# Performance work log

Measured on AMD Instinct MI355X. Metric: run time of the kernel, lower is better.

## Reference

```python
import jax, jax.numpy as jnp
import numpy as np

B, LQ, LK, NF = 8, 8192, 1024, 64


def setup_inputs() -> dict:
    key = jax.random.key(0)
    k1, k2, k3, k4, k5 = jax.random.split(key, 5)
    x = jax.random.normal(k1, (B, LQ, NF), dtype=jnp.float32)
    kv = jax.random.normal(k2, (B, LK, NF), dtype=jnp.float32)
    # 1x1 submanifold convolutions == per-point linear maps (no bias)
    scale = 1.0 / np.sqrt(NF)
    Wq = jax.random.normal(k3, (NF, NF), dtype=jnp.float32) * scale
    Wk = jax.random.normal(k4, (NF, NF), dtype=jnp.float32) * scale
    Wv = jax.random.normal(k5, (NF, NF), dtype=jnp.float32) * scale
    return {"x": x, "kv": kv, "Wq": Wq, "Wk": Wk, "Wv": Wv}


def reference(x, kv, Wq, Wk, Wv):
    # q/k/v projections (1x1 convs on sparse features = dense matmuls)
    q = jnp.einsum("bqd,de->bqe", x, Wq)    # [B, LQ, NF]
    k = jnp.einsum("bkd,de->bke", kv, Wk)   # [B, LK, NF]
    v = jnp.einsum("bkd,de->bke", kv, Wv)   # [B, LK, NF]
    # per-batch (block-diagonal / ragged) attention: e = q k^T, softmax over keys, @ v
    scores = jnp.einsum("bqe,bke->bqk", q, k)        # [B, LQ, LK] (no scaling, as in source)
    attn = jax.nn.softmax(scores, axis=-1)
    out = jnp.einsum("bqk,bke->bqe", attn, v)        # [B, LQ, NF]
    return out
```

## Files before the change

### kernel.cpp

```cpp
#include <hip/hip_runtime.h>
#include <hip/hip_fp16.h>

constexpr int B_  = 8;
constexpr int LQ  = 8192;
constexpr int LK  = 1024;
constexpr int NF  = 64;

typedef _Float16 f16x8  __attribute__((ext_vector_type(8)));
typedef float    f32x16 __attribute__((ext_vector_type(16)));

#define MFMA32(a, b, c) __builtin_amdgcn_mfma_f32_32x32x16_f16((a), (b), (c), 0, 0, 0)

__device__ __forceinline__ f16x8 ldf(const _Float16* p) { return *(const f16x8*)p; }

__device__ __forceinline__ f16x8 ldfrag_f32(const float* row, int t, int h) {
  int off = 32 * (t >> 1) + 16 * (t & 1) + 4 * h;
  float4 r0 = *(const float4*)(row + off);
  float4 r1 = *(const float4*)(row + off + 8);
  f16x8 r;
  r[0] = (_Float16)r0.x; r[1] = (_Float16)r0.y; r[2] = (_Float16)r0.z; r[3] = (_Float16)r0.w;
  r[4] = (_Float16)r1.x; r[5] = (_Float16)r1.y; r[6] = (_Float16)r1.z; r[7] = (_Float16)r1.w;
  return r;
}

__device__ __forceinline__ f16x8 pk8(const f32x16 c, int u) {
  int b = u * 8;
  auto p0 = __builtin_amdgcn_cvt_pkrtz(c[b],     c[b + 1]);
  auto p1 = __builtin_amdgcn_cvt_pkrtz(c[b + 2], c[b + 3]);
  auto p2 = __builtin_amdgcn_cvt_pkrtz(c[b + 4], c[b + 5]);
  auto p3 = __builtin_amdgcn_cvt_pkrtz(c[b + 6], c[b + 7]);
  f16x8 r;
  r[0] = p0[0]; r[1] = p0[1]; r[2] = p1[0]; r[3] = p1[1];
  r[4] = p2[0]; r[5] = p2[1]; r[6] = p3[0]; r[7] = p3[1];
  return r;
}

__device__ __forceinline__ int w_src_idx(int idx) {
  int chunk = idx >> 9, r9 = idx & 511;
  int lane_ = r9 >> 3, j = r9 & 7;
  int m32 = lane_ & 31, h = lane_ >> 5;
  int tt = chunk & 3;
  int din  = 32 * (tt >> 1) + 16 * (tt & 1) + 4 * h + 8 * (j >> 2) + (j & 3);
  int dout = (chunk >> 2) * 32 + m32;
  return din * 64 + dout;
}

__device__ __forceinline__ void dma16(const _Float16* g, _Float16* l) {
  __builtin_amdgcn_global_load_lds(
      (const __attribute__((address_space(1))) unsigned int*)g,
      (__attribute__((address_space(3))) unsigned int*)l, 16, 0, 0);
}

__device__ __forceinline__ void tile_barrier() {
  asm volatile("s_waitcnt vmcnt(0)\n\ts_barrier" ::: "memory");
}

__global__ __launch_bounds__(256) void kv_proj_kernel(
    const float* __restrict__ kv, const float* __restrict__ Wk,
    const float* __restrict__ Wv, _Float16* __restrict__ KV) {
  __shared__ __align__(16) _Float16 wlds[8192];

  const int t    = threadIdx.x;
  const int wave = t >> 6, lane = t & 63, m32 = lane & 31, h = lane >> 5;
  const int bb   = blockIdx.x >> 3;
  const int kblk = blockIdx.x & 7;

#pragma unroll
  for (int i = 0; i < 16; ++i) {
    int idx = t + 256 * i;
    int s = w_src_idx(idx);
    wlds[idx]        = (_Float16)Wk[s];
    wlds[4096 + idx] = (_Float16)Wv[s];
  }

  const int key = kblk * 128 + wave * 32 + m32;
  const float* kvrow = kv + ((size_t)bb * LK + key) * NF;
  f16x8 kvf[4];
#pragma unroll
  for (int tt = 0; tt < 4; ++tt) kvf[tt] = ldfrag_f32(kvrow, tt, h);
  __syncthreads();

  const int T = bb * 16 + kblk * 2 + (wave >> 1);
  _Float16* tile = KV + (size_t)T * 8192;
  const int kb = wave & 1;

#pragma unroll
  for (int mb = 0; mb < 2; ++mb) {
    f32x16 C = {};
#pragma unroll
    for (int tt = 0; tt < 4; ++tt)
      C = MFMA32(ldf(&wlds[(mb * 4 + tt) * 512 + lane * 8]), kvf[tt], C);
#pragma unroll
    for (int u = 0; u < 2; ++u)
      *(f16x8*)(tile + ((size_t)(kb * 4 + 2 * mb + u)) * 512 + lane * 8) = pk8(C, u);
  }
#pragma unroll
  for (int nb = 0; nb < 2; ++nb) {
    f32x16 C = {};
#pragma unroll
    for (int tt = 0; tt < 4; ++tt)
      C = MFMA32(kvf[tt], ldf(&wlds[4096 + (nb * 4 + tt) * 512 + lane * 8]), C);
#pragma unroll
    for (int u = 0; u < 2; ++u)
      *(f16x8*)(tile + 4096 + ((size_t)(nb * 4 + 2 * kb + u)) * 512 + lane * 8) = pk8(C, u);
  }
}

__global__ __launch_bounds__(256, 1) void attn_kernel(
    const float* __restrict__ x, const float* __restrict__ Wq,
    const _Float16* __restrict__ KV, float* __restrict__ out) {
  __shared__ __align__(16) _Float16 lds[2 * 8192 + 4096];

  const int t    = threadIdx.x;
  const int wave = t >> 6, lane = t & 63, m32 = lane & 31, h = lane >> 5;
  const int b    = blockIdx.x >> 5;
  const int qw_base = (blockIdx.x & 31) * 256 + wave * 64;
  constexpr float LOG2E = 1.44269504088896f;

  _Float16* wq_l = lds + 16384;
#pragma unroll
  for (int i = 0; i < 16; ++i) {
    int idx = t + 256 * i;
    wq_l[idx] = (_Float16)(Wq[w_src_idx(idx)] * LOG2E);
  }

  const _Float16* KVb = KV + (size_t)b * 16 * 8192;
#pragma unroll
  for (int q = 0; q < 4; ++q) {
    int ch = wave * 4 + q;
    dma16(KVb + ch * 512 + lane * 8, lds + ch * 512);
  }
  __syncthreads();

  f16x8 qb[2][4];
  {
    f16x8 wa[2][4];
#pragma unroll
    for (int mb = 0; mb < 2; ++mb)
#pragma unroll
      for (int tt = 0; tt < 4; ++tt)
        wa[mb][tt] = ldf(&wq_l[(mb * 4 + tt) * 512 + lane * 8]);
#pragma unroll
    for (int s = 0; s < 2; ++s) {
      const float* xrow = x + ((size_t)b * LQ + qw_base + s * 32 + m32) * NF;
      f16x8 xf[4];
#pragma unroll
      for (int tt = 0; tt < 4; ++tt) xf[tt] = ldfrag_f32(xrow, tt, h);
#pragma unroll
      for (int mb = 0; mb < 2; ++mb) {
        f32x16 C = {};
#pragma unroll
        for (int tt = 0; tt < 4; ++tt) C = MFMA32(wa[mb][tt], xf[tt], C);
        qb[s][2 * mb]     = pk8(C, 0);
        qb[s][2 * mb + 1] = pk8(C, 1);
      }
    }
  }

  f16x8 ones;
#pragma unroll
  for (int j = 0; j < 8; ++j) ones[j] = (_Float16)1.0f;

  float  m_s[2] = {-1e30f, -1e30f};
  f32x16 lacc[2] = {};
  f32x16 oacc[2][2] = {};

  for (int tile = 0; tile < 16; ++tile) {
    tile_barrier();
    if (tile < 15) {
      const _Float16* nt = KVb + (size_t)(tile + 1) * 8192;
      _Float16* nb_ = lds + ((tile + 1) & 1) * 8192;
#pragma unroll
      for (int q = 0; q < 4; ++q) {
        int ch = wave * 4 + q;
        dma16(nt + ch * 512 + lane * 8, nb_ + ch * 512);
      }
    }
    const _Float16* tb = lds + (tile & 1) * 8192;

    f32x16 st[2][2] = {};
#pragma unroll
    for (int kb = 0; kb < 2; ++kb)
#pragma unroll
      for (int tt = 0; tt < 4; ++tt) {
        f16x8 a = ldf(tb + (size_t)(kb * 4 + tt) * 512 + lane * 8);
        st[0][kb] = MFMA32(a, qb[0][tt], st[0][kb]);
        st[1][kb] = MFMA32(a, qb[1][tt], st[1][kb]);
      }

    f16x8 pa[2][4];
#pragma unroll
    for (int s = 0; s < 2; ++s) {
      float tmax = st[s][0][0];
#pragma unroll
      for (int kb = 0; kb < 2; ++kb)
#pragma unroll
        for (int r = 1 - kb; r < 16; ++r) tmax = fmaxf(tmax, st[s][kb][r]);
      tmax = fmaxf(tmax, __shfl_xor(tmax, 32));

      if (__ballot(tmax > m_s[s]) != 0) {
        float mnew  = fmaxf(m_s[s], tmax);
        float alpha = __builtin_amdgcn_exp2f(m_s[s] - mnew);
        m_s[s] = mnew;
        float ar[16];
#pragma unroll
        for (int r = 0; r < 16; ++r)
          ar[r] = __shfl(alpha, (r & 3) + 8 * (r >> 2) + 4 * h);
#pragma unroll
        for (int r = 0; r < 16; ++r) {
          lacc[s][r]    *= ar[r];
          oacc[s][0][r] *= ar[r];
          oacc[s][1][r] *= ar[r];
        }
      }

#pragma unroll
      for (int kb = 0; kb < 2; ++kb)
#pragma unroll
        for (int r = 0; r < 16; ++r)
          st[s][kb][r] = __builtin_amdgcn_exp2f(st[s][kb][r] - m_s[s]);

#pragma unroll
      for (int kb = 0; kb < 2; ++kb) {
        pa[s][2 * kb]     = pk8(st[s][kb], 0);
        pa[s][2 * kb + 1] = pk8(st[s][kb], 1);
      }
#pragma unroll
      for (int tt = 0; tt < 4; ++tt) lacc[s] = MFMA32(pa[s][tt], ones, lacc[s]);
    }

#pragma unroll
    for (int nb = 0; nb < 2; ++nb)
#pragma unroll
      for (int tt = 0; tt < 4; ++tt) {
        f16x8 vb = ldf(tb + 4096 + (size_t)(nb * 4 + tt) * 512 + lane * 8);
        oacc[0][nb] = MFMA32(pa[0][tt], vb, oacc[0][nb]);
        oacc[1][nb] = MFMA32(pa[1][tt], vb, oacc[1][nb]);
      }
  }

#pragma unroll
  for (int s = 0; s < 2; ++s)
#pragma unroll
    for (int r = 0; r < 16; ++r) {
      float linv = 1.0f / lacc[s][r];
      int q_out = qw_base + s * 32 + (r & 3) + 8 * (r >> 2) + 4 * h;
      float* orow = out + ((size_t)b * LQ + q_out) * NF + m32;
      orow[0]  = oacc[s][0][r] * linv;
      orow[32] = oacc[s][1][r] * linv;
    }
}

extern "C" void kernel_launch(void* const* d_in, const int* in_sizes, int n_in,
                              void* d_out, int out_size, void* d_ws, size_t ws_size,
                              hipStream_t stream) {
  const float* x  = (const float*)d_in[0];
  const float* kv = (const float*)d_in[1];
  const float* Wq = (const float*)d_in[2];
  const float* Wk = (const float*)d_in[3];
  const float* Wv = (const float*)d_in[4];
  float* out = (float*)d_out;

  _Float16* KV = (_Float16*)d_ws;

  kv_proj_kernel<<<B_ * (LK / 128), 256, 0, stream>>>(kv, Wk, Wv, KV);
  attn_kernel<<<B_ * (LQ / 256), 256, 0, stream>>>(x, Wq, KV, out);
}
```

Before: 116.2 us.

## Split key range across two wave groups per block and merge softmax states

Attention blocks grow from 256 to 512 threads. Two groups of four waves each process half of the key tiles (8 tiles each) for the same 256 queries, with separate double-buffered LDS regions. At the end the partial max, row-sum and output accumulators from group 1 go through LDS and group 0 merges them flash-decoding style before writing. The aim is to halve the serial key loop per wave and raise occupancy, at the cost of more LDS, an extra merge phase and duplicated Q projection work in both groups.

```diff
diff --git a/kernel.cpp b/kernel.cpp
--- a/kernel.cpp
+++ b/kernel.cpp
@@ -106,29 +106,30 @@
   }
 }
 
-__global__ __launch_bounds__(256, 1) void attn_kernel(
+__global__ __launch_bounds__(512, 2) void attn_kernel(
     const float* __restrict__ x, const float* __restrict__ Wq,
     const _Float16* __restrict__ KV, float* __restrict__ out) {
-  __shared__ __align__(16) _Float16 lds[2 * 8192 + 4096];
+  __shared__ __align__(16) _Float16 lds[2][2][8192];
+  __shared__ __align__(16) _Float16 wq_l[4096];
 
   const int t    = threadIdx.x;
   const int wave = t >> 6, lane = t & 63, m32 = lane & 31, h = lane >> 5;
+  const int wq_i = wave & 3, wg = wave >> 2;
   const int b    = blockIdx.x >> 5;
-  const int qw_base = (blockIdx.x & 31) * 256 + wave * 64;
+  const int qw_base = (blockIdx.x & 31) * 256 + wq_i * 64;
   constexpr float LOG2E = 1.44269504088896f;
 
-  _Float16* wq_l = lds + 16384;
-#pragma unroll
-  for (int i = 0; i < 16; ++i) {
-    int idx = t + 256 * i;
+#pragma unroll
+  for (int i = 0; i < 8; ++i) {
+    int idx = t + 512 * i;
     wq_l[idx] = (_Float16)(Wq[w_src_idx(idx)] * LOG2E);
   }
 
-  const _Float16* KVb = KV + (size_t)b * 16 * 8192;
+  const _Float16* Kg = KV + ((size_t)b * 16 + wg * 8) * 8192;
 #pragma unroll
   for (int q = 0; q < 4; ++q) {
-    int ch = wave * 4 + q;
-    dma16(KVb + ch * 512 + lane * 8, lds + ch * 512);
+    int ch = wq_i * 4 + q;
+    dma16(Kg + ch * 512 + lane * 8, &lds[wg][0][ch * 512]);
   }
   __syncthreads();
 
@@ -165,18 +166,18 @@
   f32x16 lacc[2] = {};
   f32x16 oacc[2][2] = {};
 
-  for (int tile = 0; tile < 16; ++tile) {
+  for (int tile = 0; tile < 8; ++tile) {
     tile_barrier();
-    if (tile < 15) {
-      const _Float16* nt = KVb + (size_t)(tile + 1) * 8192;
-      _Float16* nb_ = lds + ((tile + 1) & 1) * 8192;
+    if (tile < 7) {
+      const _Float16* nt = Kg + (size_t)(tile + 1) * 8192;
+      _Float16* nb_ = &lds[wg][(tile + 1) & 1][0];
 #pragma unroll
       for (int q = 0; q < 4; ++q) {
-        int ch = wave * 4 + q;
+        int ch = wq_i * 4 + q;
         dma16(nt + ch * 512 + lane * 8, nb_ + ch * 512);
       }
     }
-    const _Float16* tb = lds + (tile & 1) * 8192;
+    const _Float16* tb = &lds[wg][tile & 1][0];
 
     f32x16 st[2][2] = {};
 #pragma unroll
@@ -239,16 +240,50 @@
       }
   }
 
-#pragma unroll
-  for (int s = 0; s < 2; ++s)
-#pragma unroll
-    for (int r = 0; r < 16; ++r) {
-      float linv = 1.0f / lacc[s][r];
-      int q_out = qw_base + s * 32 + (r & 3) + 8 * (r >> 2) + 4 * h;
-      float* orow = out + ((size_t)b * LQ + q_out) * NF + m32;
-      orow[0]  = oacc[s][0][r] * linv;
-      orow[32] = oacc[s][1][r] * linv;
-    }
+  float* mrg_m = (float*)&lds[0][0][0];
+  float* mrg_l = mrg_m + 256;
+  float* mrg_o = mrg_l + 4096;
+
+#pragma unroll
+  for (int s = 0; s < 2; ++s) {
+    __syncthreads();
+    if (wg == 1) {
+      mrg_m[wq_i * 64 + lane] = m_s[s];
+#pragma unroll
+      for (int r = 0; r < 16; ++r)
+        mrg_l[(wq_i * 16 + r) * 64 + lane] = lacc[s][r];
+#pragma unroll
+      for (int nb = 0; nb < 2; ++nb)
+#pragma unroll
+        for (int r = 0; r < 16; ++r)
+          mrg_o[(wq_i * 32 + nb * 16 + r) * 64 + lane] = oacc[s][nb][r];
+    }
+    __syncthreads();
+    if (wg == 0) {
+      float mh = mrg_m[wq_i * 64 + lane];
+      float mx = fmaxf(m_s[s], mh);
+      float al = __builtin_amdgcn_exp2f(m_s[s] - mx);
+      float ah = __builtin_amdgcn_exp2f(mh - mx);
+      float alr[16], ahr[16];
+#pragma unroll
+      for (int r = 0; r < 16; ++r) {
+        int src = (r & 3) + 8 * (r >> 2) + 4 * h;
+        alr[r] = __shfl(al, src);
+        ahr[r] = __shfl(ah, src);
+      }
+#pragma unroll
+      for (int r = 0; r < 16; ++r) {
+        float lh = mrg_l[(wq_i * 16 + r) * 64 + lane];
+        float linv = 1.0f / (alr[r] * lacc[s][r] + ahr[r] * lh);
+        int q_out = qw_base + s * 32 + (r & 3) + 8 * (r >> 2) + 4 * h;
+        float* orow = out + ((size_t)b * LQ + q_out) * NF + m32;
+        float o0 = alr[r] * oacc[s][0][r] + ahr[r] * mrg_o[(wq_i * 32 + r) * 64 + lane];
+        float o1 = alr[r] * oacc[s][1][r] + ahr[r] * mrg_o[(wq_i * 32 + 16 + r) * 64 + lane];
+        orow[0]  = o0 * linv;
+        orow[32] = o1 * linv;
+      }
+    }
+  }
 }
 
 extern "C" void kernel_launch(void* const* d_in, const int* in_sizes, int n_in,
@@ -264,5 +299,5 @@
   _Float16* KV = (_Float16*)d_ws;
 
   kv_proj_kernel<<<B_ * (LK / 128), 256, 0, stream>>>(kv, Wk, Wv, KV);
-  attn_kernel<<<B_ * (LQ / 256), 256, 0, stream>>>(x, Wq, KV, out);
-}
+  attn_kernel<<<B_ * (LQ / 256), 512, 0, stream>>>(x, Wq, KV, out);
+}
```

Result: faster. 111.9 us (-3.7%).

## Split keys across waves, drop online max, use bf16 P·V with LDS merge

Applied to the files above, without the earlier changes.

Restructures attention so each block handles 64 queries, with wave pairs splitting the key range and merging partial sums and outputs through LDS. Removes the running-max rescaling entirely, relying on bf16/fp32 exponent range to avoid overflow, and stores V and P in bf16. Launch bounds are raised to allow four blocks per CU. It trades numerical safety for large scores and precision of P and V for fewer VALU, shuffle and branch operations per tile.

```diff
diff --git a/kernel.cpp b/kernel.cpp
--- a/kernel.cpp
+++ b/kernel.cpp
@@ -6,12 +6,16 @@
 constexpr int LK  = 1024;
 constexpr int NF  = 64;
 
-typedef _Float16 f16x8  __attribute__((ext_vector_type(8)));
-typedef float    f32x16 __attribute__((ext_vector_type(16)));
-
-#define MFMA32(a, b, c) __builtin_amdgcn_mfma_f32_32x32x16_f16((a), (b), (c), 0, 0, 0)
+typedef _Float16     f16x8  __attribute__((ext_vector_type(8)));
+typedef short        s16x8  __attribute__((ext_vector_type(8)));
+typedef unsigned int u32x4  __attribute__((ext_vector_type(4)));
+typedef float        f32x16 __attribute__((ext_vector_type(16)));
+
+#define MFMA32F(a, b, c) __builtin_amdgcn_mfma_f32_32x32x16_f16((a), (b), (c), 0, 0, 0)
+#define MFMA32B(a, b, c) __builtin_amdgcn_mfma_f32_32x32x16_bf16((a), (b), (c), 0, 0, 0)
 
 __device__ __forceinline__ f16x8 ldf(const _Float16* p) { return *(const f16x8*)p; }
+__device__ __forceinline__ s16x8 ldb(const _Float16* p) { return *(const s16x8*)p; }
 
 __device__ __forceinline__ f16x8 ldfrag_f32(const float* row, int t, int h) {
   int off = 32 * (t >> 1) + 16 * (t & 1) + 4 * h;
@@ -35,6 +39,22 @@
   return r;
 }
 
+__device__ __forceinline__ unsigned int bpack(float a, float b) {
+  unsigned int ua = __builtin_bit_cast(unsigned int, a) + 0x8000u;
+  unsigned int ub = __builtin_bit_cast(unsigned int, b) + 0x8000u;
+  return __builtin_amdgcn_perm(ub, ua, 0x07060302u);
+}
+
+__device__ __forceinline__ s16x8 pk8b(const f32x16 c, int u) {
+  int b = u * 8;
+  u32x4 r;
+  r[0] = bpack(c[b],     c[b + 1]);
+  r[1] = bpack(c[b + 2], c[b + 3]);
+  r[2] = bpack(c[b + 4], c[b + 5]);
+  r[3] = bpack(c[b + 6], c[b + 7]);
+  return __builtin_bit_cast(s16x8, r);
+}
+
 __device__ __forceinline__ int w_src_idx(int idx) {
   int chunk = idx >> 9, r9 = idx & 511;
   int lane_ = r9 >> 3, j = r9 & 7;
@@ -80,175 +100,135 @@
   for (int tt = 0; tt < 4; ++tt) kvf[tt] = ldfrag_f32(kvrow, tt, h);
   __syncthreads();
 
-  const int T = bb * 16 + kblk * 2 + (wave >> 1);
-  _Float16* tile = KV + (size_t)T * 8192;
-  const int kb = wave & 1;
+  _Float16* base = KV + ((size_t)bb * 32 + kblk * 4 + wave) * 4096;
 
 #pragma unroll
   for (int mb = 0; mb < 2; ++mb) {
     f32x16 C = {};
 #pragma unroll
     for (int tt = 0; tt < 4; ++tt)
-      C = MFMA32(ldf(&wlds[(mb * 4 + tt) * 512 + lane * 8]), kvf[tt], C);
+      C = MFMA32F(ldf(&wlds[(mb * 4 + tt) * 512 + lane * 8]), kvf[tt], C);
 #pragma unroll
     for (int u = 0; u < 2; ++u)
-      *(f16x8*)(tile + ((size_t)(kb * 4 + 2 * mb + u)) * 512 + lane * 8) = pk8(C, u);
+      *(f16x8*)(base + (size_t)(2 * mb + u) * 512 + lane * 8) = pk8(C, u);
   }
 #pragma unroll
   for (int nb = 0; nb < 2; ++nb) {
     f32x16 C = {};
 #pragma unroll
     for (int tt = 0; tt < 4; ++tt)
-      C = MFMA32(kvf[tt], ldf(&wlds[4096 + (nb * 4 + tt) * 512 + lane * 8]), C);
+      C = MFMA32F(kvf[tt], ldf(&wlds[4096 + (nb * 4 + tt) * 512 + lane * 8]), C);
 #pragma unroll
     for (int u = 0; u < 2; ++u)
-      *(f16x8*)(tile + 4096 + ((size_t)(nb * 4 + 2 * kb + u)) * 512 + lane * 8) = pk8(C, u);
-  }
-}
-
-__global__ __launch_bounds__(256, 1) void attn_kernel(
+      *(s16x8*)(base + 2048 + (size_t)(nb * 2 + u) * 512 + lane * 8) = pk8b(C, u);
+  }
+}
+
+__global__ __launch_bounds__(256, 4) void attn_kernel(
     const float* __restrict__ x, const float* __restrict__ Wq,
     const _Float16* __restrict__ KV, float* __restrict__ out) {
-  __shared__ __align__(16) _Float16 lds[2 * 8192 + 4096];
+  __shared__ __align__(16) _Float16 lds[4][4096];
 
   const int t    = threadIdx.x;
   const int wave = t >> 6, lane = t & 63, m32 = lane & 31, h = lane >> 5;
-  const int b    = blockIdx.x >> 5;
-  const int qw_base = (blockIdx.x & 31) * 256 + wave * 64;
+  const int kg   = wave & 1, qg = wave >> 1;
+  const int b    = blockIdx.x >> 7;
+  const int q_base = (blockIdx.x & 127) * 64;
   constexpr float LOG2E = 1.44269504088896f;
 
-  _Float16* wq_l = lds + 16384;
 #pragma unroll
   for (int i = 0; i < 16; ++i) {
     int idx = t + 256 * i;
-    wq_l[idx] = (_Float16)(Wq[w_src_idx(idx)] * LOG2E);
-  }
-
-  const _Float16* KVb = KV + (size_t)b * 16 * 8192;
+    lds[1][idx] = (_Float16)(Wq[w_src_idx(idx)] * LOG2E);
+  }
+
+  const _Float16* Kg = KV + ((size_t)b * 32 + kg * 16) * 4096;
 #pragma unroll
   for (int q = 0; q < 4; ++q) {
-    int ch = wave * 4 + q;
-    dma16(KVb + ch * 512 + lane * 8, lds + ch * 512);
-  }
-  __syncthreads();
-
-  f16x8 qb[2][4];
+    int ch = qg * 4 + q;
+    dma16(Kg + ch * 512 + lane * 8, &lds[kg * 2][ch * 512]);
+  }
+  __syncthreads();
+
+  f16x8 qb[4];
   {
-    f16x8 wa[2][4];
-#pragma unroll
-    for (int mb = 0; mb < 2; ++mb)
+    const float* xrow = x + ((size_t)b * LQ + q_base + qg * 32 + m32) * NF;
+    f16x8 xf[4];
+#pragma unroll
+    for (int tt = 0; tt < 4; ++tt) xf[tt] = ldfrag_f32(xrow, tt, h);
+#pragma unroll
+    for (int mb = 0; mb < 2; ++mb) {
+      f32x16 C = {};
 #pragma unroll
       for (int tt = 0; tt < 4; ++tt)
-        wa[mb][tt] = ldf(&wq_l[(mb * 4 + tt) * 512 + lane * 8]);
-#pragma unroll
-    for (int s = 0; s < 2; ++s) {
-      const float* xrow = x + ((size_t)b * LQ + qw_base + s * 32 + m32) * NF;
-      f16x8 xf[4];
-#pragma unroll
-      for (int tt = 0; tt < 4; ++tt) xf[tt] = ldfrag_f32(xrow, tt, h);
-#pragma unroll
-      for (int mb = 0; mb < 2; ++mb) {
-        f32x16 C = {};
-#pragma unroll
-        for (int tt = 0; tt < 4; ++tt) C = MFMA32(wa[mb][tt], xf[tt], C);
-        qb[s][2 * mb]     = pk8(C, 0);
-        qb[s][2 * mb + 1] = pk8(C, 1);
-      }
-    }
-  }
-
-  f16x8 ones;
-#pragma unroll
-  for (int j = 0; j < 8; ++j) ones[j] = (_Float16)1.0f;
-
-  float  m_s[2] = {-1e30f, -1e30f};
-  f32x16 lacc[2] = {};
-  f32x16 oacc[2][2] = {};
-
+        C = MFMA32F(ldf(&lds[1][(mb * 4 + tt) * 512 + lane * 8]), xf[tt], C);
+      qb[2 * mb]     = pk8(C, 0);
+      qb[2 * mb + 1] = pk8(C, 1);
+    }
+  }
+
+  const u32x4 onesu = {0x3F803F80u, 0x3F803F80u, 0x3F803F80u, 0x3F803F80u};
+  const s16x8 ones = __builtin_bit_cast(s16x8, onesu);
+
+  f32x16 lacc = {};
+  f32x16 oacc[2] = {};
+
+#pragma unroll 2
   for (int tile = 0; tile < 16; ++tile) {
     tile_barrier();
     if (tile < 15) {
-      const _Float16* nt = KVb + (size_t)(tile + 1) * 8192;
-      _Float16* nb_ = lds + ((tile + 1) & 1) * 8192;
+      const _Float16* nt = Kg + (size_t)(tile + 1) * 4096;
+      _Float16* dst = &lds[kg * 2 + ((tile + 1) & 1)][0];
 #pragma unroll
       for (int q = 0; q < 4; ++q) {
-        int ch = wave * 4 + q;
-        dma16(nt + ch * 512 + lane * 8, nb_ + ch * 512);
+        int ch = qg * 4 + q;
+        dma16(nt + ch * 512 + lane * 8, dst + ch * 512);
       }
     }
-    const _Float16* tb = lds + (tile & 1) * 8192;
-
-    f32x16 st[2][2] = {};
-#pragma unroll
-    for (int kb = 0; kb < 2; ++kb)
-#pragma unroll
-      for (int tt = 0; tt < 4; ++tt) {
-        f16x8 a = ldf(tb + (size_t)(kb * 4 + tt) * 512 + lane * 8);
-        st[0][kb] = MFMA32(a, qb[0][tt], st[0][kb]);
-        st[1][kb] = MFMA32(a, qb[1][tt], st[1][kb]);
-      }
-
-    f16x8 pa[2][4];
-#pragma unroll
-    for (int s = 0; s < 2; ++s) {
-      float tmax = st[s][0][0];
-#pragma unroll
-      for (int kb = 0; kb < 2; ++kb)
-#pragma unroll
-        for (int r = 1 - kb; r < 16; ++r) tmax = fmaxf(tmax, st[s][kb][r]);
-      tmax = fmaxf(tmax, __shfl_xor(tmax, 32));
-
-      if (__ballot(tmax > m_s[s]) != 0) {
-        float mnew  = fmaxf(m_s[s], tmax);
-        float alpha = __builtin_amdgcn_exp2f(m_s[s] - mnew);
-        m_s[s] = mnew;
-        float ar[16];
-#pragma unroll
-        for (int r = 0; r < 16; ++r)
-          ar[r] = __shfl(alpha, (r & 3) + 8 * (r >> 2) + 4 * h);
-#pragma unroll
-        for (int r = 0; r < 16; ++r) {
-          lacc[s][r]    *= ar[r];
-          oacc[s][0][r] *= ar[r];
-          oacc[s][1][r] *= ar[r];
-        }
-      }
-
-#pragma unroll
-      for (int kb = 0; kb < 2; ++kb)
-#pragma unroll
-        for (int r = 0; r < 16; ++r)
-          st[s][kb][r] = __builtin_amdgcn_exp2f(st[s][kb][r] - m_s[s]);
-
-#pragma unroll
-      for (int kb = 0; kb < 2; ++kb) {
-        pa[s][2 * kb]     = pk8(st[s][kb], 0);
-        pa[s][2 * kb + 1] = pk8(st[s][kb], 1);
-      }
-#pragma unroll
-      for (int tt = 0; tt < 4; ++tt) lacc[s] = MFMA32(pa[s][tt], ones, lacc[s]);
-    }
-
-#pragma unroll
-    for (int nb = 0; nb < 2; ++nb)
-#pragma unroll
-      for (int tt = 0; tt < 4; ++tt) {
-        f16x8 vb = ldf(tb + 4096 + (size_t)(nb * 4 + tt) * 512 + lane * 8);
-        oacc[0][nb] = MFMA32(pa[0][tt], vb, oacc[0][nb]);
-        oacc[1][nb] = MFMA32(pa[1][tt], vb, oacc[1][nb]);
-      }
-  }
-
-#pragma unroll
-  for (int s = 0; s < 2; ++s)
+    const _Float16* tb = &lds[kg * 2 + (tile & 1)][0];
+
+    f32x16 st = {};
+#pragma unroll
+    for (int tt = 0; tt < 4; ++tt)
+      st = MFMA32F(ldf(tb + tt * 512 + lane * 8), qb[tt], st);
+
+#pragma unroll
+    for (int r = 0; r < 16; ++r) st[r] = __builtin_amdgcn_exp2f(st[r]);
+
+    s16x8 pa0 = pk8b(st, 0), pa1 = pk8b(st, 1);
+
+    lacc = MFMA32B(pa0, ones, lacc);
+    lacc = MFMA32B(pa1, ones, lacc);
+
+#pragma unroll
+    for (int nb = 0; nb < 2; ++nb) {
+      oacc[nb] = MFMA32B(pa0, ldb(tb + 2048 + (nb * 2 + 0) * 512 + lane * 8), oacc[nb]);
+      oacc[nb] = MFMA32B(pa1, ldb(tb + 2048 + (nb * 2 + 1) * 512 + lane * 8), oacc[nb]);
+    }
+  }
+
+  __syncthreads();
+  float* mrg = (float*)&lds[0][0];
+  const int slot = qg * 3072;
+  if (kg == 1) {
 #pragma unroll
     for (int r = 0; r < 16; ++r) {
-      float linv = 1.0f / lacc[s][r];
-      int q_out = qw_base + s * 32 + (r & 3) + 8 * (r >> 2) + 4 * h;
+      mrg[slot +        r * 64 + lane] = lacc[r];
+      mrg[slot + 1024 + r * 64 + lane] = oacc[0][r];
+      mrg[slot + 2048 + r * 64 + lane] = oacc[1][r];
+    }
+  }
+  __syncthreads();
+  if (kg == 0) {
+#pragma unroll
+    for (int r = 0; r < 16; ++r) {
+      float linv = 1.0f / (lacc[r] + mrg[slot + r * 64 + lane]);
+      int q_out = q_base + qg * 32 + (r & 3) + 8 * (r >> 2) + 4 * h;
       float* orow = out + ((size_t)b * LQ + q_out) * NF + m32;
-      orow[0]  = oacc[s][0][r] * linv;
-      orow[32] = oacc[s][1][r] * linv;
-    }
+      orow[0]  = (oacc[0][r] + mrg[slot + 1024 + r * 64 + lane]) * linv;
+      orow[32] = (oacc[1][r] + mrg[slot + 2048 + r * 64 + lane]) * linv;
+    }
+  }
 }
 
 extern "C" void kernel_launch(void* const* d_in, const int* in_sizes, int n_in,
@@ -264,5 +244,5 @@
   _Float16* KV = (_Float16*)d_ws;
 
   kv_proj_kernel<<<B_ * (LK / 128), 256, 0, stream>>>(kv, Wk, Wv, KV);
-  attn_kernel<<<B_ * (LQ / 256), 256, 0, stream>>>(x, Wq, KV, out);
-}
+  attn_kernel<<<B_ * (LQ / 64), 256, 0, stream>>>(x, Wq, KV, out);
+}
```

New measurement: 107.5 us. 1.08x faster.
